# Kernel optimization log

Hardware: AMD Instinct MI355X
Metric: run time of the kernel (lower is better)

Reference implementation:

```python
import jax, jax.numpy as jnp
import numpy as np

N_NODES = 100000
N_EDGES = 1000000
N_GRAPHS = 128
BN_EPS = 1e-5


def setup_inputs() -> dict:
    key = jax.random.key(0)
    ks = jax.random.split(key, 20)
    H = 64
    F = 128
    C = 10
    inp = {
        'x': jax.random.normal(ks[0], (N_NODES, F), jnp.float32),
        'edge_index': jax.random.randint(ks[1], (2, N_EDGES), 0, N_NODES, jnp.int64),
        'batch': jax.random.randint(ks[2], (N_NODES,), 0, N_GRAPHS, jnp.int64),
        'W1_0': jax.random.normal(ks[3], (F, H), jnp.float32) * 0.05,
        'bn_g_0': jax.random.uniform(ks[4], (H,), jnp.float32) + 0.5,
        'bn_b_0': jax.random.normal(ks[5], (H,), jnp.float32) * 0.1,
        'bn_m_0': jax.random.normal(ks[6], (H,), jnp.float32) * 0.1,
        'bn_v_0': jax.random.uniform(ks[7], (H,), jnp.float32) + 0.5,
        'W2_0': jax.random.normal(ks[8], (H, H), jnp.float32) * 0.1,
        'W1_r': jax.random.normal(ks[9], (3, H, H), jnp.float32) * 0.1,
        'bn_g_r': jax.random.uniform(ks[10], (3, H), jnp.float32) + 0.5,
        'bn_b_r': jax.random.normal(ks[11], (3, H), jnp.float32) * 0.1,
        'bn_m_r': jax.random.normal(ks[12], (3, H), jnp.float32) * 0.1,
        'bn_v_r': jax.random.uniform(ks[13], (3, H), jnp.float32) + 0.5,
        'W2_r': jax.random.normal(ks[14], (3, H, H), jnp.float32) * 0.1,
        'lin1_W': jax.random.normal(ks[15], (H, H), jnp.float32) * 0.1,
        'lin2_W': jax.random.normal(ks[16], (H, C), jnp.float32) * 0.1,
        'lin2_b': jax.random.normal(ks[17], (C,), jnp.float32) * 0.1,
    }
    return inp


def _gin_conv(x, src, dst, W1, g, b, m, v, W2):
    # sum aggregation of neighbor messages (PyG GINConv, eps=0)
    agg = jax.ops.segment_sum(x[src], dst, num_segments=N_NODES)
    h = (x + agg) @ W1                           # [N, H], Linear no bias
    h = (h - m) * jax.lax.rsqrt(v + BN_EPS) * g + b  # BatchNorm1d (eval)
    h = jax.nn.relu(h)
    h = jax.nn.relu(h @ W2)
    return h


def reference(x, edge_index, batch, W1_0, bn_g_0, bn_b_0, bn_m_0, bn_v_0, W2_0,
              W1_r, bn_g_r, bn_b_r, bn_m_r, bn_v_r, W2_r, lin1_W, lin2_W, lin2_b):
    src, dst = edge_index[0], edge_index[1]
    h = _gin_conv(x, src, dst, W1_0, bn_g_0, bn_b_0, bn_m_0, bn_v_0, W2_0)
    for i in range(W1_r.shape[0]):
        h = _gin_conv(h, src, dst, W1_r[i], bn_g_r[i], bn_b_r[i], bn_m_r[i], bn_v_r[i], W2_r[i])
    # global mean pool over graphs
    sums = jax.ops.segment_sum(h, batch, num_segments=N_GRAPHS)
    cnts = jax.ops.segment_sum(jnp.ones((h.shape[0], 1), h.dtype), batch, num_segments=N_GRAPHS)
    pooled = sums / jnp.maximum(cnts, 1.0)
    z = jax.nn.relu(pooled @ lin1_W)  # dropout inactive (eval)
    z = z @ lin2_W + lin2_b
    return jax.nn.log_softmax(z, axis=-1)
```

## Files before the change

### kernel.cpp

```cpp
#include <hip/hip_runtime.h>
#include <hip/hip_bf16.h>
#include <hip/hip_fp16.h>

#define HDIM 64
#define NGRAPH 128
#define NCLS 10
#define BN_EPS 1e-5f
#define SCAN_CHUNK 1024
#define LDH 72

typedef _Float16 h16;
typedef __attribute__((ext_vector_type(8))) _Float16 f16x8;
typedef __attribute__((ext_vector_type(4))) float f32x4;


__global__ void count_kernel(const int* __restrict__ dst, int* __restrict__ deg, int E) {
    int e = blockIdx.x * blockDim.x + threadIdx.x;
    if (e < E) atomicAdd(&deg[dst[e]], 1);
}

__global__ void scan1_kernel(const int* __restrict__ deg, int* __restrict__ part, int N) {
    __shared__ int sh[256];
    int base = blockIdx.x * SCAN_CHUNK + threadIdx.x * 4;
    int s = 0;
#pragma unroll
    for (int i = 0; i < 4; i++) { int idx = base + i; if (idx < N) s += deg[idx]; }
    sh[threadIdx.x] = s; __syncthreads();
    for (int off = 128; off > 0; off >>= 1) {
        if (threadIdx.x < off) sh[threadIdx.x] += sh[threadIdx.x + off];
        __syncthreads();
    }
    if (threadIdx.x == 0) part[blockIdx.x] = sh[0];
}

__global__ void scan2_kernel(int* __restrict__ part, int nblk, int* __restrict__ row_ptr, int N, int E) {
    __shared__ int sh[256];
    int v = (threadIdx.x < nblk) ? part[threadIdx.x] : 0;
    sh[threadIdx.x] = v; __syncthreads();
    for (int off = 1; off < 256; off <<= 1) {
        int t = (threadIdx.x >= off) ? sh[threadIdx.x - off] : 0;
        __syncthreads();
        sh[threadIdx.x] += t;
        __syncthreads();
    }
    if (threadIdx.x < nblk) part[threadIdx.x] = sh[threadIdx.x] - v;
    if (threadIdx.x == 0) row_ptr[N] = E;
}

__global__ void scan3_kernel(const int* __restrict__ deg, const int* __restrict__ part,
                             int* __restrict__ row_ptr, int* __restrict__ cursor, int N) {
    __shared__ int sh[256];
    int tbase = blockIdx.x * SCAN_CHUNK + threadIdx.x * 4;
    int vals[4]; int s = 0;
#pragma unroll
    for (int i = 0; i < 4; i++) { int idx = tbase + i; vals[i] = (idx < N) ? deg[idx] : 0; s += vals[i]; }
    sh[threadIdx.x] = s; __syncthreads();
    for (int off = 1; off < 256; off <<= 1) {
        int t = (threadIdx.x >= off) ? sh[threadIdx.x - off] : 0;
        __syncthreads();
        sh[threadIdx.x] += t;
        __syncthreads();
    }
    int run = part[blockIdx.x] + sh[threadIdx.x] - s;
#pragma unroll
    for (int i = 0; i < 4; i++) {
        int idx = tbase + i;
        if (idx < N) { row_ptr[idx] = run; cursor[idx] = run; run += vals[i]; }
    }
}


__global__ void prep_weights_kernel(const float* __restrict__ W2_0,
                                    const float* __restrict__ W2r,
                                    const float* __restrict__ W1r,
                                    h16* __restrict__ wt) {
    int b = blockIdx.x;
    const float* src = (b == 0) ? W2_0 : (b <= 3) ? W2r + (size_t)(b - 1) * 4096
                                                  : W1r + (size_t)(b - 4) * 4096;
    h16* dst = wt + (size_t)b * 4096;
    for (int i = threadIdx.x; i < 4096; i += 256) {
        int k = i >> 6, j = i & 63;
        dst[j * 64 + k] = (h16)src[k * 64 + j];
    }
}


__global__ void __launch_bounds__(256) fused_scatter_gemm0_kernel(
        const int* __restrict__ src, const int* __restrict__ dst,
        int* __restrict__ cursor, int* __restrict__ col, int E, int eb,
        const float* __restrict__ X, const float* __restrict__ W,
        __half* __restrict__ Y, int N) {
    __shared__ float Xs[64 * 64];
    __shared__ float Ws[64 * 64];

    if ((int)blockIdx.x < eb) {
        int e = blockIdx.x * 256 + threadIdx.x;
        if (e < E) {
            int pos = atomicAdd(&cursor[dst[e]], 1);
            col[pos] = src[e];
        }
        return;
    }

    const int tid = threadIdx.x;
    const int base = (blockIdx.x - eb) * 64;
    const int ti = tid >> 4;
    const int tj = tid & 15;
    float4 acc[4];
#pragma unroll
    for (int a = 0; a < 4; a++) acc[a] = make_float4(0.f, 0.f, 0.f, 0.f);

    for (int kh = 0; kh < 2; kh++) {
        {
            const float4* Wv = reinterpret_cast<const float4*>(W + kh * 64 * 64);
            float4* Wsv = reinterpret_cast<float4*>(Ws);
            for (int i = tid; i < 1024; i += 256) Wsv[i] = Wv[i];
        }
        for (int i = tid; i < 1024; i += 256) {
            int r = i & 63;
            int c4 = i >> 6;
            int n = base + r;
            float4 v = make_float4(0.f, 0.f, 0.f, 0.f);
            if (n < N) v = *reinterpret_cast<const float4*>(X + (size_t)n * 128 + kh * 64 + c4 * 4);
            Xs[(c4 * 4 + 0) * 64 + r] = v.x;
            Xs[(c4 * 4 + 1) * 64 + r] = v.y;
            Xs[(c4 * 4 + 2) * 64 + r] = v.z;
            Xs[(c4 * 4 + 3) * 64 + r] = v.w;
        }
        __syncthreads();

#pragma unroll 4
        for (int k = 0; k < 64; k++) {
            float4 xv = *reinterpret_cast<const float4*>(&Xs[k * 64 + 4 * ti]);
            float4 wv = *reinterpret_cast<const float4*>(&Ws[k * 64 + 4 * tj]);
            acc[0].x += xv.x * wv.x; acc[0].y += xv.x * wv.y; acc[0].z += xv.x * wv.z; acc[0].w += xv.x * wv.w;
            acc[1].x += xv.y * wv.x; acc[1].y += xv.y * wv.y; acc[1].z += xv.y * wv.z; acc[1].w += xv.y * wv.w;
            acc[2].x += xv.z * wv.x; acc[2].y += xv.z * wv.y; acc[2].z += xv.z * wv.z; acc[2].w += xv.z * wv.w;
            acc[3].x += xv.w * wv.x; acc[3].y += xv.w * wv.y; acc[3].z += xv.w * wv.z; acc[3].w += xv.w * wv.w;
        }
        __syncthreads();
    }

#pragma unroll
    for (int a = 0; a < 4; a++) {
        int n = base + 4 * ti + a;
        if (n < N) {
            __half2* yp = reinterpret_cast<__half2*>(Y + (size_t)n * 64 + 4 * tj);
            yp[0] = __floats2half2_rn(acc[a].x, acc[a].y);
            yp[1] = __floats2half2_rn(acc[a].z, acc[a].w);
        }
    }
}


__global__ void __launch_bounds__(256) gemm_pair_mfma(const float* __restrict__ H,
                                                      const h16* __restrict__ Wt2,
                                                      const h16* __restrict__ Wt1,
                                                      __half* __restrict__ Y, int N) {
    __shared__ h16 Xs[64 * LDH];
    __shared__ h16 W2s[64 * LDH];
    __shared__ h16 W1s[64 * LDH];
    const int tid = threadIdx.x;
    const int base = blockIdx.x * 64;

#pragma unroll
    for (int it = 0; it < 4; ++it) {
        int idx = it * 256 + tid;
        int row = idx >> 4, q = idx & 15;
        float4 v = make_float4(0.f, 0.f, 0.f, 0.f);
        int n = base + row;
        if (n < N) v = *reinterpret_cast<const float4*>(H + (size_t)n * 64 + q * 4);
        h16* d = &Xs[row * LDH + q * 4];
        d[0] = (h16)v.x; d[1] = (h16)v.y; d[2] = (h16)v.z; d[3] = (h16)v.w;
    }
#pragma unroll
    for (int it = 0; it < 2; ++it) {
        int idx = it * 256 + tid;
        int row = idx >> 3, q = idx & 7;
        *reinterpret_cast<f16x8*>(&W2s[row * LDH + q * 8]) =
            *reinterpret_cast<const f16x8*>(Wt2 + row * 64 + q * 8);
        *reinterpret_cast<f16x8*>(&W1s[row * LDH + q * 8]) =
            *reinterpret_cast<const f16x8*>(Wt1 + row * 64 + q * 8);
    }
    __syncthreads();

    const int w  = tid >> 6;
    const int l  = tid & 63;
    const int lr = l & 15;
    const int lk = l >> 4;

    f16x8 a0 = *reinterpret_cast<const f16x8*>(&Xs[(16 * w + lr) * LDH + lk * 8]);
    f16x8 a1 = *reinterpret_cast<const f16x8*>(&Xs[(16 * w + lr) * LDH + 32 + lk * 8]);
    f32x4 acc[4];
#pragma unroll
    for (int t = 0; t < 4; ++t) {
        f16x8 b0 = *reinterpret_cast<const f16x8*>(&W2s[(16 * t + lr) * LDH + lk * 8]);
        f16x8 b1 = *reinterpret_cast<const f16x8*>(&W2s[(16 * t + lr) * LDH + 32 + lk * 8]);
        f32x4 c = {0.f, 0.f, 0.f, 0.f};
        c = __builtin_amdgcn_mfma_f32_16x16x32_f16(a0, b0, c, 0, 0, 0);
        c = __builtin_amdgcn_mfma_f32_16x16x32_f16(a1, b1, c, 0, 0, 0);
        acc[t] = c;
    }
#pragma unroll
    for (int t = 0; t < 4; ++t)
#pragma unroll
        for (int r = 0; r < 4; ++r)
            Xs[(16 * w + lk * 4 + r) * LDH + 16 * t + lr] = (h16)fmaxf(acc[t][r], 0.f);
    __syncthreads();

    f16x8 z0 = *reinterpret_cast<const f16x8*>(&Xs[(16 * w + lr) * LDH + lk * 8]);
    f16x8 z1 = *reinterpret_cast<const f16x8*>(&Xs[(16 * w + lr) * LDH + 32 + lk * 8]);
    f32x4 acc2[4];
#pragma unroll
    for (int t = 0; t < 4; ++t) {
        f16x8 b0 = *reinterpret_cast<const f16x8*>(&W1s[(16 * t + lr) * LDH + lk * 8]);
        f16x8 b1 = *reinterpret_cast<const f16x8*>(&W1s[(16 * t + lr) * LDH + 32 + lk * 8]);
        f32x4 c = {0.f, 0.f, 0.f, 0.f};
        c = __builtin_amdgcn_mfma_f32_16x16x32_f16(z0, b0, c, 0, 0, 0);
        c = __builtin_amdgcn_mfma_f32_16x16x32_f16(z1, b1, c, 0, 0, 0);
        acc2[t] = c;
    }
#pragma unroll
    for (int t = 0; t < 4; ++t)
#pragma unroll
        for (int r = 0; r < 4; ++r)
            W2s[(16 * w + lk * 4 + r) * LDH + 16 * t + lr] = (h16)acc2[t][r];
    __syncthreads();

#pragma unroll
    for (int it = 0; it < 2; ++it) {
        int idx = it * 256 + tid;
        int row = idx >> 3, q = idx & 7;
        int n = base + row;
        if (n < N)
            *reinterpret_cast<f16x8*>(reinterpret_cast<h16*>(Y) + (size_t)n * 64 + q * 8) =
                *reinterpret_cast<const f16x8*>(&W2s[row * LDH + q * 8]);
    }
}


__global__ void __launch_bounds__(256) gemm_last_mfma(const float* __restrict__ H,
                                                      const h16* __restrict__ Wt,
                                                      float* __restrict__ Y, int N) {
    __shared__ h16 Xs[64 * LDH];
    __shared__ h16 Ws[64 * LDH];
    __shared__ float Zf[64 * 68];
    const int tid = threadIdx.x;
    const int base = blockIdx.x * 64;

#pragma unroll
    for (int it = 0; it < 4; ++it) {
        int idx = it * 256 + tid;
        int row = idx >> 4, q = idx & 15;
        float4 v = make_float4(0.f, 0.f, 0.f, 0.f);
        int n = base + row;
        if (n < N) v = *reinterpret_cast<const float4*>(H + (size_t)n * 64 + q * 4);
        h16* d = &Xs[row * LDH + q * 4];
        d[0] = (h16)v.x; d[1] = (h16)v.y; d[2] = (h16)v.z; d[3] = (h16)v.w;
    }
#pragma unroll
    for (int it = 0; it < 2; ++it) {
        int idx = it * 256 + tid;
        int row = idx >> 3, q = idx & 7;
        *reinterpret_cast<f16x8*>(&Ws[row * LDH + q * 8]) =
            *reinterpret_cast<const f16x8*>(Wt + row * 64 + q * 8);
    }
    __syncthreads();

    const int w  = tid >> 6;
    const int l  = tid & 63;
    const int lr = l & 15;
    const int lk = l >> 4;

    f16x8 a0 = *reinterpret_cast<const f16x8*>(&Xs[(16 * w + lr) * LDH + lk * 8]);
    f16x8 a1 = *reinterpret_cast<const f16x8*>(&Xs[(16 * w + lr) * LDH + 32 + lk * 8]);
#pragma unroll
    for (int t = 0; t < 4; ++t) {
        f16x8 b0 = *reinterpret_cast<const f16x8*>(&Ws[(16 * t + lr) * LDH + lk * 8]);
        f16x8 b1 = *reinterpret_cast<const f16x8*>(&Ws[(16 * t + lr) * LDH + 32 + lk * 8]);
        f32x4 c = {0.f, 0.f, 0.f, 0.f};
        c = __builtin_amdgcn_mfma_f32_16x16x32_f16(a0, b0, c, 0, 0, 0);
        c = __builtin_amdgcn_mfma_f32_16x16x32_f16(a1, b1, c, 0, 0, 0);
#pragma unroll
        for (int r = 0; r < 4; ++r)
            Zf[(16 * w + lk * 4 + r) * 68 + 16 * t + lr] = fmaxf(c[r], 0.f);
    }
    __syncthreads();

#pragma unroll
    for (int it = 0; it < 4; ++it) {
        int idx = it * 256 + tid;
        int row = idx >> 4, q = idx & 15;
        int n = base + row;
        if (n < N)
            *reinterpret_cast<float4*>(Y + (size_t)n * 64 + q * 4) =
                *reinterpret_cast<const float4*>(&Zf[row * 68 + q * 4]);
    }
}


__global__ void agg_bn_relu_kernel(const __half* __restrict__ y, const int* __restrict__ rp,
                                   const int* __restrict__ col,
                                   const float* __restrict__ gam, const float* __restrict__ bet,
                                   const float* __restrict__ mu, const float* __restrict__ var,
                                   float* __restrict__ out, int N) {
    int wid = (blockIdx.x * blockDim.x + threadIdx.x) >> 6;
    int lane = threadIdx.x & 63;
    if (wid >= N) return;
    int grp = lane >> 5;
    int fl  = lane & 31;
    int beg = rp[wid], end = rp[wid + 1];

    float2 acc = make_float2(0.f, 0.f);
    if (grp == 0) {
        float2 f = __half22float2(*reinterpret_cast<const __half2*>(y + (size_t)wid * 64 + fl * 2));
        acc.x += f.x; acc.y += f.y;
    }
    int e = beg + grp;
    for (; e + 6 < end; e += 8) {
        int s0 = col[e], s1 = col[e + 2], s2 = col[e + 4], s3 = col[e + 6];
        float2 a0 = __half22float2(*reinterpret_cast<const __half2*>(y + (size_t)s0 * 64 + fl * 2));
        float2 a1 = __half22float2(*reinterpret_cast<const __half2*>(y + (size_t)s1 * 64 + fl * 2));
        float2 a2 = __half22float2(*reinterpret_cast<const __half2*>(y + (size_t)s2 * 64 + fl * 2));
        float2 a3 = __half22float2(*reinterpret_cast<const __half2*>(y + (size_t)s3 * 64 + fl * 2));
        acc.x += a0.x + a1.x + a2.x + a3.x;
        acc.y += a0.y + a1.y + a2.y + a3.y;
    }
    for (; e < end; e += 2) {
        float2 a = __half22float2(*reinterpret_cast<const __half2*>(y + (size_t)col[e] * 64 + fl * 2));
        acc.x += a.x; acc.y += a.y;
    }

    acc.x += __shfl_down(acc.x, 32);
    acc.y += __shfl_down(acc.y, 32);

    if (grp == 0) {
        int f0 = fl * 2, f1 = f0 + 1;
        float sc0 = gam[f0] * rsqrtf(var[f0] + BN_EPS);
        float sc1 = gam[f1] * rsqrtf(var[f1] + BN_EPS);
        float2 o;
        o.x = fmaxf(acc.x * sc0 + (bet[f0] - mu[f0] * sc0), 0.f);
        o.y = fmaxf(acc.y * sc1 + (bet[f1] - mu[f1] * sc1), 0.f);
        *reinterpret_cast<float2*>(out + (size_t)wid * 64 + f0) = o;
    }
}


__global__ void __launch_bounds__(256) pool_partial_kernel(const float* __restrict__ h,
                                                           const int* __restrict__ batch,
                                                           float* __restrict__ partial,
                                                           int* __restrict__ pcnt, int N) {
    __shared__ float ls[NGRAPH * 64];
    __shared__ int lc[NGRAPH];
    for (int i = threadIdx.x; i < NGRAPH * 64; i += 256) ls[i] = 0.f;
    if (threadIdx.x < NGRAPH) lc[threadIdx.x] = 0;
    __syncthreads();
    int lane = threadIdx.x & 63;
    int gwave = blockIdx.x * 4 + (threadIdx.x >> 6);
    int nwaves = gridDim.x * 4;
#pragma unroll 4
    for (int n = gwave; n < N; n += nwaves) {
        int g = batch[n];
        atomicAdd(&ls[g * 64 + lane], h[(size_t)n * 64 + lane]);
        if (lane == 0) atomicAdd(&lc[g], 1);
    }
    __syncthreads();
    for (int i = threadIdx.x; i < NGRAPH * 64; i += 256)
        partial[(size_t)blockIdx.x * NGRAPH * 64 + i] = ls[i];
    if (threadIdx.x < NGRAPH) pcnt[blockIdx.x * NGRAPH + threadIdx.x] = lc[threadIdx.x];
}


__global__ void head_kernel(const float* __restrict__ partial, const int* __restrict__ pcnt, int P,
                            const float* __restrict__ lin1, const float* __restrict__ lin2,
                            const float* __restrict__ b2, float* __restrict__ out) {
    int g = blockIdx.x;
    int j = threadIdx.x;
    __shared__ float p[64];
    __shared__ float z1[64];
    __shared__ float z2[NCLS];
    __shared__ int csh[64];
    float s = 0.f;
    for (int b = 0; b < P; b++) s += partial[(size_t)b * NGRAPH * 64 + g * 64 + j];
    int c = 0;
    for (int b = j; b < P; b += 64) c += pcnt[b * NGRAPH + g];
    csh[j] = c; __syncthreads();
    if (j == 0) { int t = 0; for (int k = 0; k < 64; k++) t += csh[k]; csh[0] = t; }
    __syncthreads();
    float cnt = fmaxf((float)csh[0], 1.f);
    p[j] = s / cnt;
    __syncthreads();
    float a = 0.f;
#pragma unroll
    for (int k = 0; k < 64; k++) a += p[k] * lin1[k * 64 + j];
    z1[j] = fmaxf(a, 0.f);
    __syncthreads();
    if (j < NCLS) {
        float t = b2[j];
#pragma unroll
        for (int k = 0; k < 64; k++) t += z1[k] * lin2[k * NCLS + j];
        z2[j] = t;
    }
    __syncthreads();
    if (j < NCLS) {
        float mx = -1e30f;
#pragma unroll
        for (int c2 = 0; c2 < NCLS; c2++) mx = fmaxf(mx, z2[c2]);
        float se = 0.f;
#pragma unroll
        for (int c2 = 0; c2 < NCLS; c2++) se += expf(z2[c2] - mx);
        out[g * NCLS + j] = z2[j] - mx - logf(se);
    }
}


extern "C" void kernel_launch(void* const* d_in, const int* in_sizes, int n_in,
                              void* d_out, int out_size, void* d_ws, size_t ws_size,
                              hipStream_t stream) {
    const float* x     = (const float*)d_in[0];
    const int*   ei    = (const int*)d_in[1];
    const int*   batch = (const int*)d_in[2];
    const float* W1_0  = (const float*)d_in[3];
    const float* g0    = (const float*)d_in[4];
    const float* b0    = (const float*)d_in[5];
    const float* m0    = (const float*)d_in[6];
    const float* v0    = (const float*)d_in[7];
    const float* W2_0  = (const float*)d_in[8];
    const float* W1r   = (const float*)d_in[9];
    const float* gr    = (const float*)d_in[10];
    const float* br    = (const float*)d_in[11];
    const float* mr    = (const float*)d_in[12];
    const float* vr    = (const float*)d_in[13];
    const float* W2r   = (const float*)d_in[14];
    const float* lin1  = (const float*)d_in[15];
    const float* lin2  = (const float*)d_in[16];
    const float* b2    = (const float*)d_in[17];

    const int N = in_sizes[0] / 128;
    const int E = in_sizes[1] / 2;
    const int* src = ei;
    const int* dst = ei + E;

    char* p = (char*)d_ws;
    auto alloc = [&](size_t bytes) -> char* {
        char* r = p;
        p += (bytes + 255) & ~(size_t)255;
        return r;
    };
    int*    deg     = (int*)alloc((size_t)N * 4);
    int*    row_ptr = (int*)alloc((size_t)(N + 1) * 4);
    int*    cursor  = (int*)alloc((size_t)N * 4);
    int*    col     = (int*)alloc((size_t)E * 4);
    int*    part    = (int*)alloc(256 * 4);
    float*  hA      = (float*)alloc((size_t)N * 64 * 4);
    __half* y16     = (__half*)alloc((size_t)N * 64 * 2);
    h16*    wt      = (h16*)alloc((size_t)7 * 4096 * 2);
    size_t used = (size_t)(p - (char*)d_ws);
    size_t per_block = ((size_t)NGRAPH * 64 * 4) + ((size_t)NGRAPH * 4) + 512;
    size_t remain = (ws_size > used) ? (ws_size - used) : 0;
    int P = (int)(remain / per_block);
    if (P > 256) P = 256;
    if (P < 1) P = 1;
    float* partial = (float*)alloc((size_t)P * NGRAPH * 64 * 4);
    int*   pcnt    = (int*)alloc((size_t)P * NGRAPH * 4);
    (void)n_in; (void)out_size;

    hipMemsetAsync(deg, 0, (size_t)N * 4, stream);

    prep_weights_kernel<<<7, 256, 0, stream>>>(W2_0, W2r, W1r, wt);
    int eb = (E + 255) / 256;
    count_kernel<<<eb, 256, 0, stream>>>(dst, deg, E);
    int nblk = (N + SCAN_CHUNK - 1) / SCAN_CHUNK;
    scan1_kernel<<<nblk, 256, 0, stream>>>(deg, part, N);
    scan2_kernel<<<1, 256, 0, stream>>>(part, nblk, row_ptr, N, E);
    scan3_kernel<<<nblk, 256, 0, stream>>>(deg, part, row_ptr, cursor, N);

    int mb = (N + 63) / 64;
    int ab = (N * 64 + 255) / 256;

    fused_scatter_gemm0_kernel<<<eb + mb, 256, 0, stream>>>(src, dst, cursor, col, E, eb,
                                                            x, W1_0, y16, N);
    agg_bn_relu_kernel<<<ab, 256, 0, stream>>>(y16, row_ptr, col, g0, b0, m0, v0, hA, N);

    gemm_pair_mfma<<<mb, 256, 0, stream>>>(hA, wt + 0 * 4096, wt + 4 * 4096, y16, N);
    agg_bn_relu_kernel<<<ab, 256, 0, stream>>>(y16, row_ptr, col, gr, br, mr, vr, hA, N);

    gemm_pair_mfma<<<mb, 256, 0, stream>>>(hA, wt + 1 * 4096, wt + 5 * 4096, y16, N);
    agg_bn_relu_kernel<<<ab, 256, 0, stream>>>(y16, row_ptr, col, gr + 64, br + 64, mr + 64, vr + 64, hA, N);

    gemm_pair_mfma<<<mb, 256, 0, stream>>>(hA, wt + 2 * 4096, wt + 6 * 4096, y16, N);
    agg_bn_relu_kernel<<<ab, 256, 0, stream>>>(y16, row_ptr, col, gr + 128, br + 128, mr + 128, vr + 128, hA, N);

    gemm_last_mfma<<<mb, 256, 0, stream>>>(hA, wt + 3 * 4096, hA, N);

    pool_partial_kernel<<<P, 256, 0, stream>>>(hA, batch, partial, pcnt, N);
    head_kernel<<<NGRAPH, 64, 0, stream>>>(partial, pcnt, P, lin1, lin2, b2, (float*)d_out);
}
```

Before: 593.2 us.

## Fuse neighbor aggregation with BN/ReLU and MFMA GEMM pair per layer

The separate aggregate+BN+ReLU kernel, which wrote fp32 activations, is merged into the following MFMA GEMM kernel. Each block now gathers neighbor rows for its 64 nodes straight into shared memory as fp16, removing the fp32 intermediate round trip and four launches. Ping-pong fp16 buffers replace the single y16 buffer. The degree count is moved into the fused gemm0 kernel and the scatter is split out after the scan. The cost is that each wave processes 16 nodes serially, which gives the gather less parallelism and latency hiding per block.

```diff
diff --git a/kernel.cpp b/kernel.cpp
--- a/kernel.cpp
+++ b/kernel.cpp
@@ -2,7 +2,6 @@
 #include <hip/hip_bf16.h>
 #include <hip/hip_fp16.h>
 
-#define HDIM 64
 #define NGRAPH 128
 #define NCLS 10
 #define BN_EPS 1e-5f
@@ -13,11 +12,6 @@
 typedef __attribute__((ext_vector_type(8))) _Float16 f16x8;
 typedef __attribute__((ext_vector_type(4))) float f32x4;
 
-
-__global__ void count_kernel(const int* __restrict__ dst, int* __restrict__ deg, int E) {
-    int e = blockIdx.x * blockDim.x + threadIdx.x;
-    if (e < E) atomicAdd(&deg[dst[e]], 1);
-}
 
 __global__ void scan1_kernel(const int* __restrict__ deg, int* __restrict__ part, int N) {
     __shared__ int sh[256];
@@ -66,6 +60,15 @@
     for (int i = 0; i < 4; i++) {
         int idx = tbase + i;
         if (idx < N) { row_ptr[idx] = run; cursor[idx] = run; run += vals[i]; }
+    }
+}
+
+__global__ void scatter_kernel(const int* __restrict__ src, const int* __restrict__ dst,
+                               int* __restrict__ cursor, int* __restrict__ col, int E) {
+    int e = blockIdx.x * blockDim.x + threadIdx.x;
+    if (e < E) {
+        int pos = atomicAdd(&cursor[dst[e]], 1);
+        col[pos] = src[e];
     }
 }
 
@@ -85,9 +88,8 @@
 }
 
 
-__global__ void __launch_bounds__(256) fused_scatter_gemm0_kernel(
-        const int* __restrict__ src, const int* __restrict__ dst,
-        int* __restrict__ cursor, int* __restrict__ col, int E, int eb,
+__global__ void __launch_bounds__(256) fused_count_gemm0_kernel(
+        const int* __restrict__ dst, int* __restrict__ deg, int E, int eb,
         const float* __restrict__ X, const float* __restrict__ W,
         __half* __restrict__ Y, int N) {
     __shared__ float Xs[64 * 64];
@@ -95,10 +97,7 @@
 
     if ((int)blockIdx.x < eb) {
         int e = blockIdx.x * 256 + threadIdx.x;
-        if (e < E) {
-            int pos = atomicAdd(&cursor[dst[e]], 1);
-            col[pos] = src[e];
-        }
+        if (e < E) atomicAdd(&deg[dst[e]], 1);
         return;
     }
 
@@ -153,26 +152,19 @@
 }
 
 
-__global__ void __launch_bounds__(256) gemm_pair_mfma(const float* __restrict__ H,
-                                                      const h16* __restrict__ Wt2,
-                                                      const h16* __restrict__ Wt1,
-                                                      __half* __restrict__ Y, int N) {
+__global__ void __launch_bounds__(256) fused_agg_pair(
+        const __half* __restrict__ yIn, const int* __restrict__ rp,
+        const int* __restrict__ col,
+        const float* __restrict__ gam, const float* __restrict__ bet,
+        const float* __restrict__ mu, const float* __restrict__ var,
+        const h16* __restrict__ Wt2, const h16* __restrict__ Wt1,
+        __half* __restrict__ yOut, int N) {
     __shared__ h16 Xs[64 * LDH];
     __shared__ h16 W2s[64 * LDH];
     __shared__ h16 W1s[64 * LDH];
     const int tid = threadIdx.x;
     const int base = blockIdx.x * 64;
 
-#pragma unroll
-    for (int it = 0; it < 4; ++it) {
-        int idx = it * 256 + tid;
-        int row = idx >> 4, q = idx & 15;
-        float4 v = make_float4(0.f, 0.f, 0.f, 0.f);
-        int n = base + row;
-        if (n < N) v = *reinterpret_cast<const float4*>(H + (size_t)n * 64 + q * 4);
-        h16* d = &Xs[row * LDH + q * 4];
-        d[0] = (h16)v.x; d[1] = (h16)v.y; d[2] = (h16)v.z; d[3] = (h16)v.w;
-    }
 #pragma unroll
     for (int it = 0; it < 2; ++it) {
         int idx = it * 256 + tid;
@@ -182,16 +174,62 @@
         *reinterpret_cast<f16x8*>(&W1s[row * LDH + q * 8]) =
             *reinterpret_cast<const f16x8*>(Wt1 + row * 64 + q * 8);
     }
-    __syncthreads();
-
-    const int w  = tid >> 6;
-    const int l  = tid & 63;
+
+    const int w   = tid >> 6;
+    const int l   = tid & 63;
+    const int grp = l >> 5;
+    const int fl  = l & 31;
+    const int f0  = fl * 2;
+
+    const float sc0 = gam[f0] * rsqrtf(var[f0] + BN_EPS);
+    const float sh0 = bet[f0] - mu[f0] * sc0;
+    const float sc1 = gam[f0 + 1] * rsqrtf(var[f0 + 1] + BN_EPS);
+    const float sh1 = bet[f0 + 1] - mu[f0 + 1] * sc1;
+
+    for (int r = 0; r < 16; ++r) {
+        int node = base + 16 * w + r;
+        float2 acc = make_float2(0.f, 0.f);
+        if (node < N) {
+            int beg = rp[node], end = rp[node + 1];
+            if (grp == 0) {
+                float2 f = __half22float2(*reinterpret_cast<const __half2*>(yIn + (size_t)node * 64 + f0));
+                acc.x += f.x; acc.y += f.y;
+            }
+            int e = beg + grp;
+            for (; e + 6 < end; e += 8) {
+                int s0 = col[e], s1 = col[e + 2], s2 = col[e + 4], s3 = col[e + 6];
+                float2 a0 = __half22float2(*reinterpret_cast<const __half2*>(yIn + (size_t)s0 * 64 + f0));
+                float2 a1 = __half22float2(*reinterpret_cast<const __half2*>(yIn + (size_t)s1 * 64 + f0));
+                float2 a2 = __half22float2(*reinterpret_cast<const __half2*>(yIn + (size_t)s2 * 64 + f0));
+                float2 a3 = __half22float2(*reinterpret_cast<const __half2*>(yIn + (size_t)s3 * 64 + f0));
+                acc.x += a0.x + a1.x + a2.x + a3.x;
+                acc.y += a0.y + a1.y + a2.y + a3.y;
+            }
+            for (; e < end; e += 2) {
+                float2 a = __half22float2(*reinterpret_cast<const __half2*>(yIn + (size_t)col[e] * 64 + f0));
+                acc.x += a.x; acc.y += a.y;
+            }
+            acc.x += __shfl_down(acc.x, 32);
+            acc.y += __shfl_down(acc.y, 32);
+        }
+        if (grp == 0) {
+            h16 v0 = (h16)0.f, v1 = (h16)0.f;
+            if (node < N) {
+                v0 = (h16)fmaxf(acc.x * sc0 + sh0, 0.f);
+                v1 = (h16)fmaxf(acc.y * sc1 + sh1, 0.f);
+            }
+            Xs[(16 * w + r) * LDH + f0]     = v0;
+            Xs[(16 * w + r) * LDH + f0 + 1] = v1;
+        }
+    }
+    __syncthreads();
+
     const int lr = l & 15;
     const int lk = l >> 4;
 
     f16x8 a0 = *reinterpret_cast<const f16x8*>(&Xs[(16 * w + lr) * LDH + lk * 8]);
     f16x8 a1 = *reinterpret_cast<const f16x8*>(&Xs[(16 * w + lr) * LDH + 32 + lk * 8]);
-    f32x4 acc[4];
+    f32x4 acc1[4];
 #pragma unroll
     for (int t = 0; t < 4; ++t) {
         f16x8 b0 = *reinterpret_cast<const f16x8*>(&W2s[(16 * t + lr) * LDH + lk * 8]);
@@ -199,13 +237,13 @@
         f32x4 c = {0.f, 0.f, 0.f, 0.f};
         c = __builtin_amdgcn_mfma_f32_16x16x32_f16(a0, b0, c, 0, 0, 0);
         c = __builtin_amdgcn_mfma_f32_16x16x32_f16(a1, b1, c, 0, 0, 0);
-        acc[t] = c;
+        acc1[t] = c;
     }
 #pragma unroll
     for (int t = 0; t < 4; ++t)
 #pragma unroll
         for (int r = 0; r < 4; ++r)
-            Xs[(16 * w + lk * 4 + r) * LDH + 16 * t + lr] = (h16)fmaxf(acc[t][r], 0.f);
+            Xs[(16 * w + lk * 4 + r) * LDH + 16 * t + lr] = (h16)fmaxf(acc1[t][r], 0.f);
     __syncthreads();
 
     f16x8 z0 = *reinterpret_cast<const f16x8*>(&Xs[(16 * w + lr) * LDH + lk * 8]);
@@ -233,15 +271,18 @@
         int row = idx >> 3, q = idx & 7;
         int n = base + row;
         if (n < N)
-            *reinterpret_cast<f16x8*>(reinterpret_cast<h16*>(Y) + (size_t)n * 64 + q * 8) =
+            *reinterpret_cast<f16x8*>(reinterpret_cast<h16*>(yOut) + (size_t)n * 64 + q * 8) =
                 *reinterpret_cast<const f16x8*>(&W2s[row * LDH + q * 8]);
     }
 }
 
 
-__global__ void __launch_bounds__(256) gemm_last_mfma(const float* __restrict__ H,
-                                                      const h16* __restrict__ Wt,
-                                                      float* __restrict__ Y, int N) {
+__global__ void __launch_bounds__(256) fused_agg_last(
+        const __half* __restrict__ yIn, const int* __restrict__ rp,
+        const int* __restrict__ col,
+        const float* __restrict__ gam, const float* __restrict__ bet,
+        const float* __restrict__ mu, const float* __restrict__ var,
+        const h16* __restrict__ Wt, float* __restrict__ hOut, int N) {
     __shared__ h16 Xs[64 * LDH];
     __shared__ h16 Ws[64 * LDH];
     __shared__ float Zf[64 * 68];
@@ -249,26 +290,62 @@
     const int base = blockIdx.x * 64;
 
 #pragma unroll
-    for (int it = 0; it < 4; ++it) {
-        int idx = it * 256 + tid;
-        int row = idx >> 4, q = idx & 15;
-        float4 v = make_float4(0.f, 0.f, 0.f, 0.f);
-        int n = base + row;
-        if (n < N) v = *reinterpret_cast<const float4*>(H + (size_t)n * 64 + q * 4);
-        h16* d = &Xs[row * LDH + q * 4];
-        d[0] = (h16)v.x; d[1] = (h16)v.y; d[2] = (h16)v.z; d[3] = (h16)v.w;
-    }
-#pragma unroll
     for (int it = 0; it < 2; ++it) {
         int idx = it * 256 + tid;
         int row = idx >> 3, q = idx & 7;
         *reinterpret_cast<f16x8*>(&Ws[row * LDH + q * 8]) =
             *reinterpret_cast<const f16x8*>(Wt + row * 64 + q * 8);
     }
-    __syncthreads();
-
-    const int w  = tid >> 6;
-    const int l  = tid & 63;
+
+    const int w   = tid >> 6;
+    const int l   = tid & 63;
+    const int grp = l >> 5;
+    const int fl  = l & 31;
+    const int f0  = fl * 2;
+
+    const float sc0 = gam[f0] * rsqrtf(var[f0] + BN_EPS);
+    const float sh0 = bet[f0] - mu[f0] * sc0;
+    const float sc1 = gam[f0 + 1] * rsqrtf(var[f0 + 1] + BN_EPS);
+    const float sh1 = bet[f0 + 1] - mu[f0 + 1] * sc1;
+
+    for (int r = 0; r < 16; ++r) {
+        int node = base + 16 * w + r;
+        float2 acc = make_float2(0.f, 0.f);
+        if (node < N) {
+            int beg = rp[node], end = rp[node + 1];
+            if (grp == 0) {
+                float2 f = __half22float2(*reinterpret_cast<const __half2*>(yIn + (size_t)node * 64 + f0));
+                acc.x += f.x; acc.y += f.y;
+            }
+            int e = beg + grp;
+            for (; e + 6 < end; e += 8) {
+                int s0 = col[e], s1 = col[e + 2], s2 = col[e + 4], s3 = col[e + 6];
+                float2 a0 = __half22float2(*reinterpret_cast<const __half2*>(yIn + (size_t)s0 * 64 + f0));
+                float2 a1 = __half22float2(*reinterpret_cast<const __half2*>(yIn + (size_t)s1 * 64 + f0));
+                float2 a2 = __half22float2(*reinterpret_cast<const __half2*>(yIn + (size_t)s2 * 64 + f0));
+                float2 a3 = __half22float2(*reinterpret_cast<const __half2*>(yIn + (size_t)s3 * 64 + f0));
+                acc.x += a0.x + a1.x + a2.x + a3.x;
+                acc.y += a0.y + a1.y + a2.y + a3.y;
+            }
+            for (; e < end; e += 2) {
+                float2 a = __half22float2(*reinterpret_cast<const __half2*>(yIn + (size_t)col[e] * 64 + f0));
+                acc.x += a.x; acc.y += a.y;
+            }
+            acc.x += __shfl_down(acc.x, 32);
+            acc.y += __shfl_down(acc.y, 32);
+        }
+        if (grp == 0) {
+            h16 v0 = (h16)0.f, v1 = (h16)0.f;
+            if (node < N) {
+                v0 = (h16)fmaxf(acc.x * sc0 + sh0, 0.f);
+                v1 = (h16)fmaxf(acc.y * sc1 + sh1, 0.f);
+            }
+            Xs[(16 * w + r) * LDH + f0]     = v0;
+            Xs[(16 * w + r) * LDH + f0 + 1] = v1;
+        }
+    }
+    __syncthreads();
+
     const int lr = l & 15;
     const int lk = l >> 4;
 
@@ -293,55 +370,8 @@
         int row = idx >> 4, q = idx & 15;
         int n = base + row;
         if (n < N)
-            *reinterpret_cast<float4*>(Y + (size_t)n * 64 + q * 4) =
+            *reinterpret_cast<float4*>(hOut + (size_t)n * 64 + q * 4) =
                 *reinterpret_cast<const float4*>(&Zf[row * 68 + q * 4]);
-    }
-}
-
-
-__global__ void agg_bn_relu_kernel(const __half* __restrict__ y, const int* __restrict__ rp,
-                                   const int* __restrict__ col,
-                                   const float* __restrict__ gam, const float* __restrict__ bet,
-                                   const float* __restrict__ mu, const float* __restrict__ var,
-                                   float* __restrict__ out, int N) {
-    int wid = (blockIdx.x * blockDim.x + threadIdx.x) >> 6;
-    int lane = threadIdx.x & 63;
-    if (wid >= N) return;
-    int grp = lane >> 5;
-    int fl  = lane & 31;
-    int beg = rp[wid], end = rp[wid + 1];
-
-    float2 acc = make_float2(0.f, 0.f);
-    if (grp == 0) {
-        float2 f = __half22float2(*reinterpret_cast<const __half2*>(y + (size_t)wid * 64 + fl * 2));
-        acc.x += f.x; acc.y += f.y;
-    }
-    int e = beg + grp;
-    for (; e + 6 < end; e += 8) {
-        int s0 = col[e], s1 = col[e + 2], s2 = col[e + 4], s3 = col[e + 6];
-        float2 a0 = __half22float2(*reinterpret_cast<const __half2*>(y + (size_t)s0 * 64 + fl * 2));
-        float2 a1 = __half22float2(*reinterpret_cast<const __half2*>(y + (size_t)s1 * 64 + fl * 2));
-        float2 a2 = __half22float2(*reinterpret_cast<const __half2*>(y + (size_t)s2 * 64 + fl * 2));
-        float2 a3 = __half22float2(*reinterpret_cast<const __half2*>(y + (size_t)s3 * 64 + fl * 2));
-        acc.x += a0.x + a1.x + a2.x + a3.x;
-        acc.y += a0.y + a1.y + a2.y + a3.y;
-    }
-    for (; e < end; e += 2) {
-        float2 a = __half22float2(*reinterpret_cast<const __half2*>(y + (size_t)col[e] * 64 + fl * 2));
-        acc.x += a.x; acc.y += a.y;
-    }
-
-    acc.x += __shfl_down(acc.x, 32);
-    acc.y += __shfl_down(acc.y, 32);
-
-    if (grp == 0) {
-        int f0 = fl * 2, f1 = f0 + 1;
-        float sc0 = gam[f0] * rsqrtf(var[f0] + BN_EPS);
-        float sc1 = gam[f1] * rsqrtf(var[f1] + BN_EPS);
-        float2 o;
-        o.x = fmaxf(acc.x * sc0 + (bet[f0] - mu[f0] * sc0), 0.f);
-        o.y = fmaxf(acc.y * sc1 + (bet[f1] - mu[f1] * sc1), 0.f);
-        *reinterpret_cast<float2*>(out + (size_t)wid * 64 + f0) = o;
     }
 }
 
@@ -453,7 +483,8 @@
     int*    col     = (int*)alloc((size_t)E * 4);
     int*    part    = (int*)alloc(256 * 4);
     float*  hA      = (float*)alloc((size_t)N * 64 * 4);
-    __half* y16     = (__half*)alloc((size_t)N * 64 * 2);
+    __half* yA      = (__half*)alloc((size_t)N * 64 * 2);
+    __half* yB      = (__half*)alloc((size_t)N * 64 * 2);
     h16*    wt      = (h16*)alloc((size_t)7 * 4096 * 2);
     size_t used = (size_t)(p - (char*)d_ws);
     size_t per_block = ((size_t)NGRAPH * 64 * 4) + ((size_t)NGRAPH * 4) + 512;
@@ -469,29 +500,22 @@
 
     prep_weights_kernel<<<7, 256, 0, stream>>>(W2_0, W2r, W1r, wt);
     int eb = (E + 255) / 256;
-    count_kernel<<<eb, 256, 0, stream>>>(dst, deg, E);
+    int mb = (N + 63) / 64;
+    fused_count_gemm0_kernel<<<eb + mb, 256, 0, stream>>>(dst, deg, E, eb, x, W1_0, yA, N);
     int nblk = (N + SCAN_CHUNK - 1) / SCAN_CHUNK;
     scan1_kernel<<<nblk, 256, 0, stream>>>(deg, part, N);
     scan2_kernel<<<1, 256, 0, stream>>>(part, nblk, row_ptr, N, E);
     scan3_kernel<<<nblk, 256, 0, stream>>>(deg, part, row_ptr, cursor, N);
-
-    int mb = (N + 63) / 64;
-    int ab = (N * 64 + 255) / 256;
-
-    fused_scatter_gemm0_kernel<<<eb + mb, 256, 0, stream>>>(src, dst, cursor, col, E, eb,
-                                                            x, W1_0, y16, N);
-    agg_bn_relu_kernel<<<ab, 256, 0, stream>>>(y16, row_ptr, col, g0, b0, m0, v0, hA, N);
-
-    gemm_pair_mfma<<<mb, 256, 0, stream>>>(hA, wt + 0 * 4096, wt + 4 * 4096, y16, N);
-    agg_bn_relu_kernel<<<ab, 256, 0, stream>>>(y16, row_ptr, col, gr, br, mr, vr, hA, N);
-
-    gemm_pair_mfma<<<mb, 256, 0, stream>>>(hA, wt + 1 * 4096, wt + 5 * 4096, y16, N);
-    agg_bn_relu_kernel<<<ab, 256, 0, stream>>>(y16, row_ptr, col, gr + 64, br + 64, mr + 64, vr + 64, hA, N);
-
-    gemm_pair_mfma<<<mb, 256, 0, stream>>>(hA, wt + 2 * 4096, wt + 6 * 4096, y16, N);
-    agg_bn_relu_kernel<<<ab, 256, 0, stream>>>(y16, row_ptr, col, gr + 128, br + 128, mr + 128, vr + 128, hA, N);
-
-    gemm_last_mfma<<<mb, 256, 0, stream>>>(hA, wt + 3 * 4096, hA, N);
+    scatter_kernel<<<eb, 256, 0, stream>>>(src, dst, cursor, col, E);
+
+    fused_agg_pair<<<mb, 256, 0, stream>>>(yA, row_ptr, col, g0, b0, m0, v0,
+                                           wt + 0 * 4096, wt + 4 * 4096, yB, N);
+    fused_agg_pair<<<mb, 256, 0, stream>>>(yB, row_ptr, col, gr, br, mr, vr,
+                                           wt + 1 * 4096, wt + 5 * 4096, yA, N);
+    fused_agg_pair<<<mb, 256, 0, stream>>>(yA, row_ptr, col, gr + 64, br + 64, mr + 64, vr + 64,
+                                           wt + 2 * 4096, wt + 6 * 4096, yB, N);
+    fused_agg_last<<<mb, 256, 0, stream>>>(yB, row_ptr, col, gr + 128, br + 128, mr + 128, vr + 128,
+                                           wt + 3 * 4096, hA, N);
 
     pool_partial_kernel<<<P, 256, 0, stream>>>(hA, batch, partial, pcnt, N);
     head_kernel<<<NGRAPH, 64, 0, stream>>>(partial, pcnt, P, lin1, lin2, b2, (float*)d_out);
```

Measured after the change: 662.8 us. 1.12x slower.
